# Kernel optimization log

Hardware: AMD Instinct MI355X
Metric: run time of the kernel (lower is better)

## Reference

```python
import jax, jax.numpy as jnp
import numpy as np

# dims
B = 2
HC, WC = 96, 96      # coarse spatial
HF, WF = 384, 384
CIN_C = 256          # in_coarser_channels
CIN_F = 3            # in_finer_channels
CH = 64              # hidden_channels
COUT = 19            # out_channels
KS, DIL = 3, 1       # local attention window


def conv2d(x, w, b=None, pad=0):
    y = jax.lax.conv_general_dilated(
        x, w, window_strides=(1, 1), padding=[(pad, pad), (pad, pad)],
        dimension_numbers=("NCHW", "OIHW", "NCHW"))
    if b is not None:
        y = y + b[None, :, None, None]
    return y


def upsample_nearest(x, factor):
    return jnp.repeat(jnp.repeat(x, factor, axis=2), factor, axis=3)


def local_attn_2d(q, k, v, kernel_size=KS, dilation=DIL):
    # per-pixel attention over a (kernel_size x kernel_size) dilated neighborhood
    Bq, C, H, W = q.shape
    Cv = v.shape[1]
    pad = dilation * (kernel_size - 1) // 2
    kp = jnp.pad(k, ((0, 0), (0, 0), (pad, pad), (pad, pad)))
    vp = jnp.pad(v, ((0, 0), (0, 0), (pad, pad), (pad, pad)))
    offs = [(i * dilation, j * dilation)
            for i in range(kernel_size) for j in range(kernel_size)]
    # scores: (B, K*K, H, W) -- q . k_neighbor per offset (zero-padded borders)
    scores = jnp.stack(
        [(q * kp[:, :, oi:oi + H, oj:oj + W]).sum(axis=1) for oi, oj in offs],
        axis=1)
    attn = jax.nn.softmax(scores, axis=1)
    y = jnp.zeros((Bq, Cv, H, W), q.dtype)
    for idx, (oi, oj) in enumerate(offs):
        y = y + attn[:, idx:idx + 1] * vp[:, :, oi:oi + H, oj:oj + W]
    return y


def setup_inputs() -> dict:
    key = jax.random.key(0)
    ks = jax.random.split(key, 11)
    p = lambda i, shape: jax.random.normal(ks[i], shape, jnp.float32) * 0.05
    return dict(
        coarse_feature=jax.random.normal(ks[0], (B, CIN_C, HC, WC), jnp.float32),
        raw_image=jax.random.uniform(ks[1], (B, CIN_F, HF, WF), jnp.float32),
        w_ef=p(2, (1, CIN_F, 3, 3)), b_ef=p(3, (1,)),          # edge_finer conv3x3
        w_ec=p(4, (CH, CIN_C, 3, 3)), b_ec=p(5, (CH,)),        # edge_coarser conv3x3
        w_eh=p(6, (1, CH + 1, 1, 1)),                          # edge_head conv1x1, no bias
        w_q=p(7, (CH, CIN_F, 1, 1)), b_q=p(8, (CH,)),          # xq_head conv1x1
        w_v=p(9, (COUT, CIN_C + CH, 1, 1)), b_v=p(10, (COUT,)) # xv_head conv1x1
    )


def reference(coarse_feature, raw_image, w_ef, b_ef, w_ec, b_ec, w_eh,
              w_q, b_q, w_v, b_v):
    f = HF // HC
    # edge branch
    ef = jax.nn.relu(conv2d(raw_image, w_ef, b_ef, pad=1))           # (B,1,HF,WF)
    ec = jax.nn.relu(conv2d(coarse_feature, w_ec, b_ec, pad=1))      # (B,CH,HC,WC)
    edge_logit = conv2d(jnp.concatenate([upsample_nearest(ec, f), ef], axis=1), w_eh)
    non_edge = jax.nn.sigmoid(edge_logit)                            # (B,1,HF,WF)
    # q / k / v
    xq = conv2d(raw_image, w_q, b_q)                                 # (B,CH,HF,WF)
    xk = non_edge * xq
    xv = conv2d(jnp.concatenate([upsample_nearest(coarse_feature, f), xq], axis=1),
                w_v, b_v)                                            # (B,COUT,HF,WF)
    y = local_attn_2d(xq, xk, xv)
    return y, non_edge
```

## Files before the change

kernel.cpp:

```cpp
#include <hip/hip_runtime.h>
#include <math.h>

#define B_    2
#define HC_   96
#define WC_   96
#define HF_   384
#define WF_   384
#define CINC_ 256
#define CH_   64
#define COUT_ 19

typedef __attribute__((ext_vector_type(8))) short bf16x8;
typedef __attribute__((ext_vector_type(4))) float f32x4;

__device__ __forceinline__ unsigned short f2bf(float f) {
    unsigned int u = __float_as_uint(f);
    u += 0x7fffu + ((u >> 16) & 1u);
    return (unsigned short)(u >> 16);
}
__device__ __forceinline__ unsigned int pk2(float a, float b) {
    return (unsigned int)f2bf(a) | ((unsigned int)f2bf(b) << 16);
}
__device__ __forceinline__ float bflo(unsigned int u) { return __uint_as_float(u << 16); }
__device__ __forceinline__ float bfhi(unsigned int u) { return __uint_as_float(u & 0xffff0000u); }

__device__ __forceinline__ void gl_lds16(const void* g, void* l) {
    __builtin_amdgcn_global_load_lds(
        (const __attribute__((address_space(1))) void*)g,
        (__attribute__((address_space(3))) void*)l, 16, 0, 0);
}

#define XT_IDX(b, chunk, hpx)  (((size_t)((b) * 32 + (chunk))) * 9604 + (hpx))

__global__ __launch_bounds__(256) void k_pre(
    const float* __restrict__ x,
    const float* __restrict__ w_ec, const float* __restrict__ w_v,
    const float* __restrict__ w_q,  const float* __restrict__ b_q,
    const float* __restrict__ b_v,
    uint4* __restrict__ Xt4,
    unsigned short* __restrict__ A_pk, unsigned short* __restrict__ Avc,
    float* __restrict__ drv)
{
    const int bid = blockIdx.x;
    const int tid = threadIdx.x;
    if (bid < 576) {
        int i = bid * 256 + tid;
        {
            int e = i & 7, l = (i >> 3) & 63, m = (i >> 9) & 3, ck = (i >> 11) & 7, tap = i >> 14;
            int oc = m * 16 + (l & 15);
            int ch = ck * 32 + (l >> 4) * 8 + e;
            A_pk[i] = f2bf(w_ec[(oc * 256 + ch) * 9 + tap]);
        }
        if (i < 8192) {
            int e = i & 7, l = (i >> 3) & 63, m = (i >> 9) & 1, ck = (i >> 10) & 7;
            int ov = m * 16 + (l & 15);
            int ch = ck * 32 + (l >> 4) * 8 + e;
            Avc[i] = (ov < COUT_) ? f2bf(w_v[ov * 320 + ch]) : (unsigned short)0;
        }
        return;
    }
    if (bid < 580) {
        int e = (bid - 576) * 256 + tid;
        if (e >= 388 * B_) return;
        int b = e / 388, i = e - b * 388;
        int gy, gx;
        if (i < 98)       { gy = 0;           gx = i; }
        else if (i < 196) { gy = 97;          gx = i - 98; }
        else if (i < 292) { gy = i - 196 + 1; gx = 0; }
        else              { gy = i - 292 + 1; gx = 97; }
        const int hpx = gy * 98 + gx;
        uint4 zz; zz.x = zz.y = zz.z = zz.w = 0u;
        #pragma unroll
        for (int c = 0; c < 32; ++c) Xt4[XT_IDX(b, c, hpx)] = zz;
        return;
    }
    if (bid < 1156) {
        int u = bid - 580;
        int bx = u % 36;
        int v2 = u / 36;
        int cg = v2 & 7;
        int b  = v2 >> 3;
        int px = bx * 256 + tid;
        int gy = px / 96, gx = px - gy * 96;
        const int hpx = (gy + 1) * 98 + gx + 1;
        const float* src = x + (size_t)b * CINC_ * 9216 + px;
        #pragma unroll
        for (int cc = 0; cc < 4; ++cc) {
            const int chunk = cg * 4 + cc;
            float f[8];
            #pragma unroll
            for (int t = 0; t < 8; ++t) f[t] = src[(size_t)(chunk * 8 + t) * 9216];
            uint4 v;
            v.x = pk2(f[0], f[1]);
            v.y = pk2(f[2], f[3]);
            v.z = pk2(f[4], f[5]);
            v.w = pk2(f[6], f[7]);
            Xt4[XT_IDX(b, chunk, hpx)] = v;
        }
        return;
    }
    {
        int i = tid;
        if (i < 9) {
            int ci = i / 3, cj = i % 3;
            float a = 0.f;
            for (int c = 0; c < 64; ++c) a += w_q[c * 3 + ci] * w_q[c * 3 + cj];
            drv[i] = a;
        } else if (i < 12) {
            int ci = i - 9;
            float a = 0.f;
            for (int c = 0; c < 64; ++c) a += w_q[c * 3 + ci] * b_q[c];
            drv[i] = a;
        } else if (i == 12) {
            float a = 0.f;
            for (int c = 0; c < 64; ++c) a += b_q[c] * b_q[c];
            drv[12] = a;
        } else if (i < 70) {
            int idx = i - 13, ci = idx / 19, ov = idx % 19;
            float a = 0.f;
            for (int c = 0; c < 64; ++c) a += w_v[ov * 320 + 256 + c] * w_q[c * 3 + ci];
            drv[i] = a;
        } else if (i < 89) {
            int ov = i - 70;
            float a = b_v[ov];
            for (int c = 0; c < 64; ++c) a += w_v[ov * 320 + 256 + c] * b_q[c];
            drv[i] = a;
        }
        return;
    }
}

__global__ __launch_bounds__(256, 2) void k_ec(
    const uint4* __restrict__ Xt4,
    const unsigned short* __restrict__ A_pk,
    const unsigned short* __restrict__ Avc,
    const float* __restrict__ b_ec, const float* __restrict__ w_eh,
    float* __restrict__ eh4,
    unsigned short* __restrict__ cvb)
{
    __shared__ uint4 sB[4][768];

    const int tid  = threadIdx.x;
    const int lane = tid & 63;
    const int wv   = tid >> 6;
    const int j    = lane & 15;
    const int g    = lane >> 4;

    const int flat = blockIdx.x;
    const int xcd  = flat & 7;
    const int slot0 = flat >> 3;
    const int z    = slot0 & 3;
    const int t8   = slot0 >> 2;
    const int tile = t8 * 8 + xcd;
    const int b    = tile / 72;
    const int tl   = tile - b * 72;
    const int ty0  = (tl / 6) * 8;
    const int tx0  = (tl % 6) * 16;

    f32x4 acc0 = (f32x4)0.f, acc1 = (f32x4)0.f;
    f32x4 accv[2][2];
    accv[0][0] = accv[0][1] = accv[1][0] = accv[1][1] = (f32x4)0.f;

    const bf16x8* Af  = (const bf16x8*)A_pk;
    const bf16x8* Avf = (const bf16x8*)Avc;

#define STAGE_EC(BUF, CK)                                                      \
    {                                                                          \
        _Pragma("unroll")                                                      \
        for (int rr = 0; rr < 3; ++rr) {                                       \
            int slot = 192 * wv + 64 * rr + lane;                              \
            int px = slot >> 2;                                                \
            px = px > 179 ? 179 : px;                                          \
            int part = (slot & 3) ^ ((px >> 1) & 3);                           \
            int row = px / 18, col = px - row * 18;                            \
            const uint4* src = Xt4 + XT_IDX(b, (CK) * 4 + part,                \
                                            (ty0 + row) * 98 + (tx0 + col));   \
            gl_lds16(src, &sB[BUF][192 * wv + 64 * rr]);                       \
        }                                                                      \
    }

    STAGE_EC(0, 0);
    STAGE_EC(1, 1);

    #pragma unroll
    for (int ck = 0; ck < 8; ++ck) {
        if (ck < 6) STAGE_EC((ck + 2) & 3, ck + 2);

        if (ck < 6)       asm volatile("s_waitcnt vmcnt(6)" ::: "memory");
        else if (ck == 6) asm volatile("s_waitcnt vmcnt(3)" ::: "memory");
        else              asm volatile("s_waitcnt vmcnt(0)" ::: "memory");
        __builtin_amdgcn_sched_barrier(0);
        asm volatile("s_barrier" ::: "memory");

        const int cur = ck & 3;
        bf16x8 frg[4][3];
        #pragma unroll
        for (int rr = 0; rr < 4; ++rr)
            #pragma unroll
            for (int dx = 0; dx < 3; ++dx) {
                int px = (2 * wv + rr) * 18 + j + dx;
                int slot = (px << 2) + (g ^ ((px >> 1) & 3));
                frg[rr][dx] = *(const bf16x8*)&sB[cur][slot];
            }

        #pragma unroll
        for (int tap = 0; tap < 9; ++tap) {
            const int dy = tap / 3, dx = tap % 3;
            bf16x8 a = Af[((tap * 8 + ck) * 4 + z) * 64 + lane];
            acc0 = __builtin_amdgcn_mfma_f32_16x16x32_bf16(a, frg[dy][dx], acc0, 0, 0, 0);
            acc1 = __builtin_amdgcn_mfma_f32_16x16x32_bf16(a, frg[dy + 1][dx], acc1, 0, 0, 0);
        }
        if (z == 0) {
            bf16x8 av0 = Avf[(ck * 2 + 0) * 64 + lane];
            bf16x8 av1 = Avf[(ck * 2 + 1) * 64 + lane];
            accv[0][0] = __builtin_amdgcn_mfma_f32_16x16x32_bf16(av0, frg[1][1], accv[0][0], 0, 0, 0);
            accv[0][1] = __builtin_amdgcn_mfma_f32_16x16x32_bf16(av0, frg[2][1], accv[0][1], 0, 0, 0);
            accv[1][0] = __builtin_amdgcn_mfma_f32_16x16x32_bf16(av1, frg[1][1], accv[1][0], 0, 0, 0);
            accv[1][1] = __builtin_amdgcn_mfma_f32_16x16x32_bf16(av1, frg[2][1], accv[1][1], 0, 0, 0);
        }
    }
#undef STAGE_EC

    float we[4], be[4];
    #pragma unroll
    for (int q = 0; q < 4; ++q) {
        int oc = z * 16 + 4 * g + q;
        we[q] = w_eh[oc];
        be[q] = b_ec[oc];
    }
    #pragma unroll
    for (int r = 0; r < 2; ++r) {
        const f32x4 accr = r ? acc1 : acc0;
        float p = 0.f;
        #pragma unroll
        for (int q = 0; q < 4; ++q)
            p += we[q] * fmaxf(accr[q] + be[q], 0.f);
        p += __shfl_xor(p, 16);
        p += __shfl_xor(p, 32);
        const int gpix = (ty0 + 2 * wv + r) * WC_ + tx0 + j;
        if (g == 0)
            eh4[((size_t)b * (HC_ * WC_) + gpix) * 4 + z] = p;
        if (z == 0) {
            unsigned short* cvp = cvb + ((size_t)b * (HC_ * WC_) + gpix) * 24;
            #pragma unroll
            for (int m = 0; m < 2; ++m)
                #pragma unroll
                for (int q = 0; q < 4; ++q) {
                    int ov = m * 16 + 4 * g + q;
                    if (ov < 20) cvp[ov] = f2bf(accv[m][r][q]);
                }
        }
    }
}

__global__ __launch_bounds__(512, 6) void k_fine(
    const float* __restrict__ raw,
    const float* __restrict__ w_ef, const float* __restrict__ b_ef,
    const float* __restrict__ w_eh,
    const float* __restrict__ drv,
    const float* __restrict__ eh4,
    const unsigned short* __restrict__ cvb,
    float* __restrict__ out_y,
    float* __restrict__ out_ne)
{
    __shared__ float sRaw[3][20][36];
    __shared__ unsigned short sV[612 * 26];
    __shared__ float sNE[612];

    const int tid = threadIdx.x;
    const int b   = blockIdx.z;
    const int ty0 = blockIdx.y * 16;
    const int tx0 = blockIdx.x * 32;
    const float* rb = raw + (size_t)b * 3 * (HF_ * WF_);

    const float* Gm = drv;
    const float* uv = drv + 9;
    const float* Mm = drv + 13;
    const float* bc = drv + 70;

    for (int i = tid; i < 2160; i += 512) {
        int ch = i / 720, rem = i - ch * 720;
        int ry = rem / 36, rx = rem - ry * 36;
        int gh = ty0 + ry - 2, gw = tx0 + rx - 2;
        float v = 0.f;
        if (gh >= 0 && gh < HF_ && gw >= 0 && gw < WF_)
            v = rb[(size_t)ch * (HF_ * WF_) + gh * WF_ + gw];
        sRaw[ch][ry][rx] = v;
    }
    __syncthreads();

    for (int p = tid; p < 612; p += 512) {
        const int iy = p / 34, ix = p - iy * 34;
        const int gh = ty0 + iy - 1, gw = tx0 + ix - 1;
        unsigned int* vw = (unsigned int*)&sV[p * 26];
        if (gh < 0 || gh >= HF_ || gw < 0 || gw >= WF_) {
            #pragma unroll
            for (int w = 0; w < 10; ++w) vw[w] = 0u;
            sNE[p] = 0.f;
            continue;
        }
        float ef = b_ef[0];
        #pragma unroll
        for (int ci = 0; ci < 3; ++ci)
            #pragma unroll
            for (int t = 0; t < 9; ++t)
                ef = fmaf(w_ef[ci * 9 + t], sRaw[ci][iy + t / 3][ix + t % 3], ef);
        ef = fmaxf(ef, 0.f);

        const int cpix = (gh >> 2) * WC_ + (gw >> 2);
        const float4 ehv = *(const float4*)(eh4 + ((size_t)b * (HC_ * WC_) + cpix) * 4);
        float logit = fmaf(w_eh[64], ef, (ehv.x + ehv.y) + (ehv.z + ehv.w));
        float ne = 1.f / (1.f + __expf(-logit));
        sNE[p] = ne;

        const float r0 = sRaw[0][iy + 1][ix + 1];
        const float r1 = sRaw[1][iy + 1][ix + 1];
        const float r2 = sRaw[2][iy + 1][ix + 1];

        float v[20];
        {
            const uint4* cvp = (const uint4*)(cvb + ((size_t)b * (HC_ * WC_) + cpix) * 24);
            uint4 a0 = cvp[0], a1 = cvp[1];
            uint4 a2 = cvp[2];
            unsigned int w10[10] = {a0.x, a0.y, a0.z, a0.w, a1.x, a1.y, a1.z, a1.w, a2.x, a2.y};
            #pragma unroll
            for (int o2 = 0; o2 < 10; ++o2) {
                v[2 * o2]     = bflo(w10[o2]);
                v[2 * o2 + 1] = bfhi(w10[o2]);
            }
        }
        #pragma unroll
        for (int ov = 0; ov < COUT_; ++ov)
            v[ov] = fmaf(Mm[38 + ov], r2,
                    fmaf(Mm[19 + ov], r1,
                    fmaf(Mm[ov], r0, v[ov] + bc[ov])));

        #pragma unroll
        for (int o2 = 0; o2 < 9; ++o2)
            vw[o2] = pk2(v[2 * o2], v[2 * o2 + 1]);
        vw[9] = (unsigned int)f2bf(v[18]);
    }
    __syncthreads();

    const int py = tid >> 5, px2 = tid & 31;
    const int iy = py + 1, ix = px2 + 1;
    const int pbase = iy * 34 + ix;

    float rn[3][9];
    #pragma unroll
    for (int ci = 0; ci < 3; ++ci)
        #pragma unroll
        for (int k = 0; k < 9; ++k)
            rn[ci][k] = sRaw[ci][iy + k / 3][ix + k % 3];

    const float rc0 = rn[0][4], rc1 = rn[1][4], rc2 = rn[2][4];
    const float h0 = fmaf(Gm[0], rc0, fmaf(Gm[1], rc1, fmaf(Gm[2], rc2, uv[0])));
    const float h1 = fmaf(Gm[3], rc0, fmaf(Gm[4], rc1, fmaf(Gm[5], rc2, uv[1])));
    const float h2 = fmaf(Gm[6], rc0, fmaf(Gm[7], rc1, fmaf(Gm[8], rc2, uv[2])));
    const float ac = fmaf(uv[0], rc0, fmaf(uv[1], rc1, fmaf(uv[2], rc2, drv[12])));

    float sc[9];
    #pragma unroll
    for (int k = 0; k < 9; ++k) {
        float d = fmaf(h0, rn[0][k], fmaf(h1, rn[1][k], fmaf(h2, rn[2][k], ac)));
        const int pn = pbase + (k / 3 - 1) * 34 + (k % 3 - 1);
        sc[k] = sNE[pn] * d;
    }
    float mmax = sc[0];
    #pragma unroll
    for (int k = 1; k < 9; ++k) mmax = fmaxf(mmax, sc[k]);
    float e[9];
    float ssum = 0.f;
    #pragma unroll
    for (int k = 0; k < 9; ++k) { e[k] = __expf(sc[k] - mmax); ssum += e[k]; }
    const float inv = 1.f / ssum;

    float y[COUT_];
    #pragma unroll
    for (int ov = 0; ov < COUT_; ++ov) y[ov] = 0.f;
    #pragma unroll
    for (int k = 0; k < 9; ++k) {
        const int pn = pbase + (k / 3 - 1) * 34 + (k % 3 - 1);
        const float a = e[k] * inv;
        const unsigned int* vp = (const unsigned int*)&sV[pn * 26];
        #pragma unroll
        for (int o2 = 0; o2 < 9; ++o2) {
            unsigned int u = vp[o2];
            y[2 * o2]     = fmaf(a, bflo(u), y[2 * o2]);
            y[2 * o2 + 1] = fmaf(a, bfhi(u), y[2 * o2 + 1]);
        }
        y[18] = fmaf(a, bflo(vp[9]), y[18]);
    }

    const int gh = ty0 + py, gw = tx0 + px2;
    const size_t ppos = (size_t)gh * WF_ + gw;
    #pragma unroll
    for (int ov = 0; ov < COUT_; ++ov)
        out_y[((size_t)b * COUT_ + ov) * (HF_ * WF_) + ppos] = y[ov];
    out_ne[(size_t)b * (HF_ * WF_) + ppos] = sNE[pbase];
}

extern "C" void kernel_launch(void* const* d_in, const int* in_sizes, int n_in,
                              void* d_out, int out_size, void* d_ws, size_t ws_size,
                              hipStream_t stream)
{
    const float* coarse = (const float*)d_in[0];
    const float* raw    = (const float*)d_in[1];
    const float* w_ef   = (const float*)d_in[2];
    const float* b_ef   = (const float*)d_in[3];
    const float* w_ec   = (const float*)d_in[4];
    const float* b_ec   = (const float*)d_in[5];
    const float* w_eh   = (const float*)d_in[6];
    const float* w_q    = (const float*)d_in[7];
    const float* b_q    = (const float*)d_in[8];
    const float* w_v    = (const float*)d_in[9];
    const float* b_v    = (const float*)d_in[10];
    (void)in_sizes; (void)n_in; (void)out_size; (void)ws_size;

    unsigned char* ws = (unsigned char*)d_ws;
    size_t off = 0;
    uint4* Xt4            = (uint4*)(ws + off);          off += (size_t)B_ * 32 * 9604 * 16;
    unsigned short* A_pk  = (unsigned short*)(ws + off); off += 294912;
    unsigned short* Avc   = (unsigned short*)(ws + off); off += 16384;
    float* eh4            = (float*)(ws + off);          off += (size_t)B_ * 9216 * 4 * 4;
    unsigned short* cvb   = (unsigned short*)(ws + off); off += (size_t)B_ * 9216 * 24 * 2;
    float* drv            = (float*)(ws + off);          off += 512;

    float* out_y  = (float*)d_out;
    float* out_ne = out_y + (size_t)B_ * COUT_ * HF_ * WF_;

    hipLaunchKernelGGL(k_pre, dim3(1157), dim3(256), 0, stream,
                       coarse, w_ec, w_v, w_q, b_q, b_v, Xt4, A_pk, Avc, drv);
    hipLaunchKernelGGL(k_ec, dim3(576), dim3(256), 0, stream,
                       Xt4, A_pk, Avc, b_ec, w_eh, eh4, cvb);
    hipLaunchKernelGGL(k_fine, dim3(12, 24, B_), dim3(512), 0, stream,
                       raw, w_ef, b_ef, w_eh, drv, eh4, cvb, out_y, out_ne);
}
```

Before: 45.52 us.

## Fuse three kernels into one persistent cooperative kernel with grid syncs

Merges the pre-pack, coarse-conv and fine attention kernels into a single cooperative persistent kernel that loops over work items and uses grid-wide syncs between phases, with a union of shared memory. The fine phase is also retiled from 16x32 tiles with 512 threads to 16x16 tiles with 256 threads to match the shared block size. The intent is to remove inter-launch gaps. The cost is grid-barrier overhead, occupancy capped by the largest phase's register and LDS usage, and a smaller fine tile with more halo overhead.

```diff
diff --git a/kernel.cpp b/kernel.cpp
--- a/kernel.cpp
+++ b/kernel.cpp
@@ -1,5 +1,8 @@
 #include <hip/hip_runtime.h>
+#include <hip/hip_cooperative_groups.h>
 #include <math.h>
+
+namespace cg = cooperative_groups;
 
 #define B_    2
 #define HC_   96
@@ -32,8 +35,10 @@
 
 #define XT_IDX(b, chunk, hpx)  (((size_t)((b) * 32 + (chunk))) * 9604 + (hpx))
 
-__global__ __launch_bounds__(256) void k_pre(
-    const float* __restrict__ x,
+
+__device__ __forceinline__ void phaseP_body(
+    int w, int tid,
+    const float* __restrict__ coarse,
     const float* __restrict__ w_ec, const float* __restrict__ w_v,
     const float* __restrict__ w_q,  const float* __restrict__ b_q,
     const float* __restrict__ b_v,
@@ -41,10 +46,8 @@
     unsigned short* __restrict__ A_pk, unsigned short* __restrict__ Avc,
     float* __restrict__ drv)
 {
-    const int bid = blockIdx.x;
-    const int tid = threadIdx.x;
-    if (bid < 576) {
-        int i = bid * 256 + tid;
+    if (w < 576) {
+        int i = w * 256 + tid;
         {
             int e = i & 7, l = (i >> 3) & 63, m = (i >> 9) & 3, ck = (i >> 11) & 7, tap = i >> 14;
             int oc = m * 16 + (l & 15);
@@ -57,36 +60,33 @@
             int ch = ck * 32 + (l >> 4) * 8 + e;
             Avc[i] = (ov < COUT_) ? f2bf(w_v[ov * 320 + ch]) : (unsigned short)0;
         }
-        return;
-    }
-    if (bid < 580) {
-        int e = (bid - 576) * 256 + tid;
-        if (e >= 388 * B_) return;
-        int b = e / 388, i = e - b * 388;
-        int gy, gx;
-        if (i < 98)       { gy = 0;           gx = i; }
-        else if (i < 196) { gy = 97;          gx = i - 98; }
-        else if (i < 292) { gy = i - 196 + 1; gx = 0; }
-        else              { gy = i - 292 + 1; gx = 97; }
-        const int hpx = gy * 98 + gx;
-        uint4 zz; zz.x = zz.y = zz.z = zz.w = 0u;
-        #pragma unroll
-        for (int c = 0; c < 32; ++c) Xt4[XT_IDX(b, c, hpx)] = zz;
-        return;
-    }
-    if (bid < 1156) {
-        int u = bid - 580;
+    } else if (w < 580) {
+        int e = (w - 576) * 256 + tid;
+        if (e < 388 * B_) {
+            int b = e / 388, i = e - b * 388;
+            int gy, gx;
+            if (i < 98)       { gy = 0;           gx = i; }
+            else if (i < 196) { gy = 97;          gx = i - 98; }
+            else if (i < 292) { gy = i - 196 + 1; gx = 0; }
+            else              { gy = i - 292 + 1; gx = 97; }
+            const int hpx = gy * 98 + gx;
+            uint4 zz; zz.x = zz.y = zz.z = zz.w = 0u;
+            #pragma unroll
+            for (int c = 0; c < 32; ++c) Xt4[XT_IDX(b, c, hpx)] = zz;
+        }
+    } else if (w < 1156) {
+        int u = w - 580;
         int bx = u % 36;
         int v2 = u / 36;
-        int cg = v2 & 7;
+        int cg2 = v2 & 7;
         int b  = v2 >> 3;
         int px = bx * 256 + tid;
         int gy = px / 96, gx = px - gy * 96;
         const int hpx = (gy + 1) * 98 + gx + 1;
-        const float* src = x + (size_t)b * CINC_ * 9216 + px;
+        const float* src = coarse + (size_t)b * CINC_ * 9216 + px;
         #pragma unroll
         for (int cc = 0; cc < 4; ++cc) {
-            const int chunk = cg * 4 + cc;
+            const int chunk = cg2 * 4 + cc;
             float f[8];
             #pragma unroll
             for (int t = 0; t < 8; ++t) f[t] = src[(size_t)(chunk * 8 + t) * 9216];
@@ -97,9 +97,7 @@
             v.w = pk2(f[6], f[7]);
             Xt4[XT_IDX(b, chunk, hpx)] = v;
         }
-        return;
-    }
-    {
+    } else {
         int i = tid;
         if (i < 9) {
             int ci = i / 3, cj = i % 3;
@@ -126,31 +124,26 @@
             for (int c = 0; c < 64; ++c) a += w_v[ov * 320 + 256 + c] * b_q[c];
             drv[i] = a;
         }
-        return;
-    }
-}
-
-__global__ __launch_bounds__(256, 2) void k_ec(
+    }
+}
+
+__device__ __forceinline__ void phaseE_body(
+    int w, int tid, uint4 (*sB)[768],
     const uint4* __restrict__ Xt4,
     const unsigned short* __restrict__ A_pk,
     const unsigned short* __restrict__ Avc,
     const float* __restrict__ b_ec, const float* __restrict__ w_eh,
-    float* __restrict__ eh4,
-    unsigned short* __restrict__ cvb)
-{
-    __shared__ uint4 sB[4][768];
-
-    const int tid  = threadIdx.x;
+    float* __restrict__ eh4, unsigned short* __restrict__ cvb)
+{
     const int lane = tid & 63;
     const int wv   = tid >> 6;
     const int j    = lane & 15;
     const int g    = lane >> 4;
 
-    const int flat = blockIdx.x;
-    const int xcd  = flat & 7;
-    const int slot0 = flat >> 3;
-    const int z    = slot0 & 3;
-    const int t8   = slot0 >> 2;
+    const int xcd  = w & 7;
+    const int sl0  = w >> 3;
+    const int z    = sl0 & 3;
+    const int t8   = sl0 >> 2;
     const int tile = t8 * 8 + xcd;
     const int b    = tile / 72;
     const int tl   = tile - b * 72;
@@ -253,24 +246,25 @@
     }
 }
 
-__global__ __launch_bounds__(512, 6) void k_fine(
+struct FineSmem {
+    float sRaw[3][20][20];
+    unsigned short sV[324 * 26];
+    float sNE[324];
+};
+
+__device__ __forceinline__ void phaseF_body(
+    int w, int tid, FineSmem* f,
     const float* __restrict__ raw,
     const float* __restrict__ w_ef, const float* __restrict__ b_ef,
-    const float* __restrict__ w_eh,
-    const float* __restrict__ drv,
-    const float* __restrict__ eh4,
-    const unsigned short* __restrict__ cvb,
-    float* __restrict__ out_y,
-    float* __restrict__ out_ne)
-{
-    __shared__ float sRaw[3][20][36];
-    __shared__ unsigned short sV[612 * 26];
-    __shared__ float sNE[612];
-
-    const int tid = threadIdx.x;
-    const int b   = blockIdx.z;
-    const int ty0 = blockIdx.y * 16;
-    const int tx0 = blockIdx.x * 32;
+    const float* __restrict__ w_eh, const float* __restrict__ drv,
+    const float* __restrict__ eh4, const unsigned short* __restrict__ cvb,
+    float* __restrict__ out_y, float* __restrict__ out_ne)
+{
+    const int bx = w % 24;
+    const int by = (w / 24) % 24;
+    const int b  = w / 576;
+    const int ty0 = by * 16;
+    const int tx0 = bx * 16;
     const float* rb = raw + (size_t)b * 3 * (HF_ * WF_);
 
     const float* Gm = drv;
@@ -278,25 +272,25 @@
     const float* Mm = drv + 13;
     const float* bc = drv + 70;
 
-    for (int i = tid; i < 2160; i += 512) {
-        int ch = i / 720, rem = i - ch * 720;
-        int ry = rem / 36, rx = rem - ry * 36;
+    for (int i = tid; i < 1200; i += 256) {
+        int ch = i / 400, rem = i - ch * 400;
+        int ry = rem / 20, rx = rem - ry * 20;
         int gh = ty0 + ry - 2, gw = tx0 + rx - 2;
         float v = 0.f;
         if (gh >= 0 && gh < HF_ && gw >= 0 && gw < WF_)
             v = rb[(size_t)ch * (HF_ * WF_) + gh * WF_ + gw];
-        sRaw[ch][ry][rx] = v;
+        f->sRaw[ch][ry][rx] = v;
     }
     __syncthreads();
 
-    for (int p = tid; p < 612; p += 512) {
-        const int iy = p / 34, ix = p - iy * 34;
+    for (int p = tid; p < 324; p += 256) {
+        const int iy = p / 18, ix = p - iy * 18;
         const int gh = ty0 + iy - 1, gw = tx0 + ix - 1;
-        unsigned int* vw = (unsigned int*)&sV[p * 26];
+        unsigned int* vw = (unsigned int*)&f->sV[p * 26];
         if (gh < 0 || gh >= HF_ || gw < 0 || gw >= WF_) {
             #pragma unroll
-            for (int w = 0; w < 10; ++w) vw[w] = 0u;
-            sNE[p] = 0.f;
+            for (int q = 0; q < 10; ++q) vw[q] = 0u;
+            f->sNE[p] = 0.f;
             continue;
         }
         float ef = b_ef[0];
@@ -304,24 +298,23 @@
         for (int ci = 0; ci < 3; ++ci)
             #pragma unroll
             for (int t = 0; t < 9; ++t)
-                ef = fmaf(w_ef[ci * 9 + t], sRaw[ci][iy + t / 3][ix + t % 3], ef);
+                ef = fmaf(w_ef[ci * 9 + t], f->sRaw[ci][iy + t / 3][ix + t % 3], ef);
         ef = fmaxf(ef, 0.f);
 
         const int cpix = (gh >> 2) * WC_ + (gw >> 2);
         const float4 ehv = *(const float4*)(eh4 + ((size_t)b * (HC_ * WC_) + cpix) * 4);
         float logit = fmaf(w_eh[64], ef, (ehv.x + ehv.y) + (ehv.z + ehv.w));
         float ne = 1.f / (1.f + __expf(-logit));
-        sNE[p] = ne;
-
-        const float r0 = sRaw[0][iy + 1][ix + 1];
-        const float r1 = sRaw[1][iy + 1][ix + 1];
-        const float r2 = sRaw[2][iy + 1][ix + 1];
+        f->sNE[p] = ne;
+
+        const float r0 = f->sRaw[0][iy + 1][ix + 1];
+        const float r1 = f->sRaw[1][iy + 1][ix + 1];
+        const float r2 = f->sRaw[2][iy + 1][ix + 1];
 
         float v[20];
         {
             const uint4* cvp = (const uint4*)(cvb + ((size_t)b * (HC_ * WC_) + cpix) * 24);
-            uint4 a0 = cvp[0], a1 = cvp[1];
-            uint4 a2 = cvp[2];
+            uint4 a0 = cvp[0], a1 = cvp[1], a2 = cvp[2];
             unsigned int w10[10] = {a0.x, a0.y, a0.z, a0.w, a1.x, a1.y, a1.z, a1.w, a2.x, a2.y};
             #pragma unroll
             for (int o2 = 0; o2 < 10; ++o2) {
@@ -342,16 +335,16 @@
     }
     __syncthreads();
 
-    const int py = tid >> 5, px2 = tid & 31;
+    const int py = tid >> 4, px2 = tid & 15;
     const int iy = py + 1, ix = px2 + 1;
-    const int pbase = iy * 34 + ix;
+    const int pbase = iy * 18 + ix;
 
     float rn[3][9];
     #pragma unroll
     for (int ci = 0; ci < 3; ++ci)
         #pragma unroll
         for (int k = 0; k < 9; ++k)
-            rn[ci][k] = sRaw[ci][iy + k / 3][ix + k % 3];
+            rn[ci][k] = f->sRaw[ci][iy + k / 3][ix + k % 3];
 
     const float rc0 = rn[0][4], rc1 = rn[1][4], rc2 = rn[2][4];
     const float h0 = fmaf(Gm[0], rc0, fmaf(Gm[1], rc1, fmaf(Gm[2], rc2, uv[0])));
@@ -363,8 +356,8 @@
     #pragma unroll
     for (int k = 0; k < 9; ++k) {
         float d = fmaf(h0, rn[0][k], fmaf(h1, rn[1][k], fmaf(h2, rn[2][k], ac)));
-        const int pn = pbase + (k / 3 - 1) * 34 + (k % 3 - 1);
-        sc[k] = sNE[pn] * d;
+        const int pn = pbase + (k / 3 - 1) * 18 + (k % 3 - 1);
+        sc[k] = f->sNE[pn] * d;
     }
     float mmax = sc[0];
     #pragma unroll
@@ -380,9 +373,9 @@
     for (int ov = 0; ov < COUT_; ++ov) y[ov] = 0.f;
     #pragma unroll
     for (int k = 0; k < 9; ++k) {
-        const int pn = pbase + (k / 3 - 1) * 34 + (k % 3 - 1);
+        const int pn = pbase + (k / 3 - 1) * 18 + (k % 3 - 1);
         const float a = e[k] * inv;
-        const unsigned int* vp = (const unsigned int*)&sV[pn * 26];
+        const unsigned int* vp = (const unsigned int*)&f->sV[pn * 26];
         #pragma unroll
         for (int o2 = 0; o2 < 9; ++o2) {
             unsigned int u = vp[o2];
@@ -397,7 +390,81 @@
     #pragma unroll
     for (int ov = 0; ov < COUT_; ++ov)
         out_y[((size_t)b * COUT_ + ov) * (HF_ * WF_) + ppos] = y[ov];
-    out_ne[(size_t)b * (HF_ * WF_) + ppos] = sNE[pbase];
+    out_ne[(size_t)b * (HF_ * WF_) + ppos] = f->sNE[pbase];
+}
+
+__global__ __launch_bounds__(256, 2) void k_all(
+    const float* __restrict__ coarse, const float* __restrict__ raw,
+    const float* __restrict__ w_ef,   const float* __restrict__ b_ef,
+    const float* __restrict__ w_ec,   const float* __restrict__ b_ec,
+    const float* __restrict__ w_eh,
+    const float* __restrict__ w_q,    const float* __restrict__ b_q,
+    const float* __restrict__ w_v,    const float* __restrict__ b_v,
+    uint4* __restrict__ Xt4,
+    unsigned short* __restrict__ A_pk, unsigned short* __restrict__ Avc,
+    float* __restrict__ eh4, unsigned short* __restrict__ cvb,
+    float* __restrict__ drv,
+    float* __restrict__ out_y, float* __restrict__ out_ne)
+{
+    __shared__ union {
+        uint4 sB[4][768];
+        FineSmem f;
+    } sm;
+
+    const int bid = blockIdx.x;
+    const int gsz = gridDim.x;
+    const int tid = threadIdx.x;
+
+    for (int w = bid; w < 1157; w += gsz)
+        phaseP_body(w, tid, coarse, w_ec, w_v, w_q, b_q, b_v, Xt4, A_pk, Avc, drv);
+
+    cg::this_grid().sync();
+
+    for (int w = bid; w < 576; w += gsz) {
+        phaseE_body(w, tid, sm.sB, Xt4, A_pk, Avc, b_ec, w_eh, eh4, cvb);
+        __syncthreads();
+    }
+
+    cg::this_grid().sync();
+
+    for (int w = bid; w < 1152; w += gsz) {
+        __syncthreads();
+        phaseF_body(w, tid, &sm.f, raw, w_ef, b_ef, w_eh, drv, eh4, cvb, out_y, out_ne);
+    }
+}
+
+__global__ __launch_bounds__(256) void k_pre(
+    const float* __restrict__ x,
+    const float* __restrict__ w_ec, const float* __restrict__ w_v,
+    const float* __restrict__ w_q,  const float* __restrict__ b_q,
+    const float* __restrict__ b_v,
+    uint4* __restrict__ Xt4,
+    unsigned short* __restrict__ A_pk, unsigned short* __restrict__ Avc,
+    float* __restrict__ drv)
+{
+    phaseP_body(blockIdx.x, threadIdx.x, x, w_ec, w_v, w_q, b_q, b_v, Xt4, A_pk, Avc, drv);
+}
+
+__global__ __launch_bounds__(256, 2) void k_ec(
+    const uint4* __restrict__ Xt4,
+    const unsigned short* __restrict__ A_pk,
+    const unsigned short* __restrict__ Avc,
+    const float* __restrict__ b_ec, const float* __restrict__ w_eh,
+    float* __restrict__ eh4, unsigned short* __restrict__ cvb)
+{
+    __shared__ uint4 sB[4][768];
+    phaseE_body(blockIdx.x, threadIdx.x, sB, Xt4, A_pk, Avc, b_ec, w_eh, eh4, cvb);
+}
+
+__global__ __launch_bounds__(256) void k_fine(
+    const float* __restrict__ raw,
+    const float* __restrict__ w_ef, const float* __restrict__ b_ef,
+    const float* __restrict__ w_eh, const float* __restrict__ drv,
+    const float* __restrict__ eh4, const unsigned short* __restrict__ cvb,
+    float* __restrict__ out_y, float* __restrict__ out_ne)
+{
+    __shared__ FineSmem f;
+    phaseF_body(blockIdx.x, threadIdx.x, &f, raw, w_ef, b_ef, w_eh, drv, eh4, cvb, out_y, out_ne);
 }
 
 extern "C" void kernel_launch(void* const* d_in, const int* in_sizes, int n_in,
@@ -429,10 +496,30 @@
     float* out_y  = (float*)d_out;
     float* out_ne = out_y + (size_t)B_ * COUT_ * HF_ * WF_;
 
-    hipLaunchKernelGGL(k_pre, dim3(1157), dim3(256), 0, stream,
-                       coarse, w_ec, w_v, w_q, b_q, b_v, Xt4, A_pk, Avc, drv);
-    hipLaunchKernelGGL(k_ec, dim3(576), dim3(256), 0, stream,
-                       Xt4, A_pk, Avc, b_ec, w_eh, eh4, cvb);
-    hipLaunchKernelGGL(k_fine, dim3(12, 24, B_), dim3(512), 0, stream,
-                       raw, w_ef, b_ef, w_eh, drv, eh4, cvb, out_y, out_ne);
-}
+    int maxPerCU = 0;
+    hipError_t occ = hipOccupancyMaxActiveBlocksPerMultiprocessor(
+        &maxPerCU, (const void*)k_all, 256, 0);
+    int grid = 512;
+    if (occ == hipSuccess && maxPerCU >= 1) {
+        grid = maxPerCU * 256;
+        if (grid > 1152) grid = 1152;
+        if (grid < 256)  grid = 256;
+    }
+
+    void* args[] = {
+        (void*)&coarse, (void*)&raw, (void*)&w_ef, (void*)&b_ef, (void*)&w_ec,
+        (void*)&b_ec,   (void*)&w_eh, (void*)&w_q, (void*)&b_q,  (void*)&w_v,
+        (void*)&b_v,    (void*)&Xt4,  (void*)&A_pk, (void*)&Avc, (void*)&eh4,
+        (void*)&cvb,    (void*)&drv,  (void*)&out_y, (void*)&out_ne
+    };
+    hipError_t e = hipLaunchCooperativeKernel((void*)k_all, dim3(grid), dim3(256),
+                                              args, 0, stream);
+    if (e != hipSuccess) {
+        hipLaunchKernelGGL(k_pre, dim3(1157), dim3(256), 0, stream,
+                           coarse, w_ec, w_v, w_q, b_q, b_v, Xt4, A_pk, Avc, drv);
+        hipLaunchKernelGGL(k_ec, dim3(576), dim3(256), 0, stream,
+                           Xt4, A_pk, Avc, b_ec, w_eh, eh4, cvb);
+        hipLaunchKernelGGL(k_fine, dim3(1152), dim3(256), 0, stream,
+                           raw, w_ef, b_ef, w_eh, drv, eh4, cvb, out_y, out_ne);
+    }
+}
```

After: 152.8 us. 3.36x slower.
